# Optimization experiments

Measured on AMD Instinct MI355X. Metric: run time of the kernel, lower is better.

## Reference

```python
import jax, jax.numpy as jnp
import numpy as np

D_IN, D_HID, D_CLS, N_CLASSES = 1024, 256, 128, 4
CELL_IN = 512
N = 50000


def setup_inputs() -> dict:
    key = jax.random.key(0)
    ks = jax.random.split(key, 20)
    s = 0.02
    inp = {
        "x_path": jax.random.normal(ks[0], (1, N, D_IN), jnp.float32),
        "x_cell": jax.random.normal(ks[1], (1, N, CELL_IN), jnp.float32),
        # wsi_net / cell_net projections
        "wsi_w": jax.random.normal(ks[2], (D_IN, D_HID), jnp.float32) * s,
        "wsi_b": jnp.zeros((D_HID,), jnp.float32),
        "cell_w": jax.random.normal(ks[3], (CELL_IN, D_HID), jnp.float32) * s,
        "cell_b": jnp.zeros((D_HID,), jnp.float32),
        # cross-attention Q/K/V
        "wq_w": jax.random.normal(ks[4], (D_HID, D_HID), jnp.float32) * s,
        "wq_b": jnp.zeros((D_HID,), jnp.float32),
        "wk_w": jax.random.normal(ks[5], (D_HID, D_HID), jnp.float32) * s,
        "wk_b": jnp.zeros((D_HID,), jnp.float32),
        "wv_w": jax.random.normal(ks[6], (D_HID, D_HID), jnp.float32) * s,
        "wv_b": jnp.zeros((D_HID,), jnp.float32),
        # gated attention (L=D=256, n_classes=1)
        "aa_w": jax.random.normal(ks[7], (D_HID, D_HID), jnp.float32) * s,
        "aa_b": jnp.zeros((D_HID,), jnp.float32),
        "ab_w": jax.random.normal(ks[8], (D_HID, D_HID), jnp.float32) * s,
        "ab_b": jnp.zeros((D_HID,), jnp.float32),
        "ac_w": jax.random.normal(ks[9], (D_HID, 1), jnp.float32) * s,
        "ac_b": jnp.zeros((1,), jnp.float32),
        # classifier MLP
        "c1_w": jax.random.normal(ks[10], (D_HID, D_CLS), jnp.float32) * s,
        "c1_b": jnp.zeros((D_CLS,), jnp.float32),
        "c2_w": jax.random.normal(ks[11], (D_CLS, N_CLASSES), jnp.float32) * s,
        "c2_b": jnp.zeros((N_CLASSES,), jnp.float32),
    }
    return inp


def reference(x_path, x_cell, wsi_w, wsi_b, cell_w, cell_b,
              wq_w, wq_b, wk_w, wk_b, wv_w, wv_b,
              aa_w, aa_b, ab_w, ab_b, ac_w, ac_b,
              c1_w, c1_b, c2_w, c2_b):
    xp = x_path[0]            # (N, D_IN)
    xc = x_cell[0]            # (N, CELL_IN)
    # instance-level projections (dropout inactive at eval)
    h_path = jax.nn.relu(xp @ wsi_w + wsi_b)    # (N, d)
    h_cell = jax.nn.relu(xc @ cell_w + cell_b)  # (N, d)
    # cross attention with per-instance seq_len=1 (bmm over N singleton batches)
    q = h_cell @ wq_w + wq_b
    k = h_path @ wk_w + wk_b
    v = h_path @ wv_w + wv_b
    scores = (jnp.einsum('nd,nd->n', q, k) / jnp.sqrt(jnp.float32(q.shape[-1])))[:, None, None]  # (N,1,1)
    attn_w = jax.nn.softmax(scores, axis=-1)     # (N,1,1), trivially ones
    fused = attn_w[:, 0, :] * v                  # (N, d)
    # gated attention MIL pooling
    a = jnp.tanh(fused @ aa_w + aa_b)
    b = jax.nn.sigmoid(fused @ ab_w + ab_b)
    A = (a * b) @ ac_w + ac_b                    # (N, 1)
    A_t = A.T                                    # (1, N)
    pooled = jax.nn.softmax(A_t, axis=1) @ fused # (1, d)
    # classifier MLP
    risk = jax.nn.relu(pooled @ c1_w + c1_b) @ c2_w + c2_b  # (1, n_classes)
    return risk
```

## Files before the change

### kernel.cpp

```cpp
#include <hip/hip_runtime.h>
#include <hip/hip_bf16.h>
#include <math.h>

#define D_IN 1024
#define D_HID 256
#define D_CLS 128
#define N_CLASSES 4
#define N_INST 50000

#define ROWS 64
#define NBLK ((N_INST + ROWS - 1) / ROWS)
#define NB2 64
#define CHUNK ((NBLK + NB2 - 1) / NB2)
#define NEG_BIG (-1e30f)

typedef __attribute__((ext_vector_type(8))) short bf16x8;
typedef __attribute__((ext_vector_type(4))) float f32x4;

__device__ __forceinline__ short f2bf(float x) {
    __hip_bfloat16 h = __float2bfloat16(x);
    return *reinterpret_cast<short*>(&h);
}

__device__ __forceinline__ float fast_tanh(float x) {
    float e = __expf(2.f * x);
    return 1.f - 2.f * __builtin_amdgcn_rcpf(e + 1.f);
}
__device__ __forceinline__ float fast_sigmoid(float x) {
    return __builtin_amdgcn_rcpf(1.f + __expf(-x));
}

__device__ __forceinline__ bf16x8 load_cvt8(const float* __restrict__ p) {
    float4 a = *(const float4*)p;
    float4 b = *(const float4*)(p + 4);
    bf16x8 r;
    r[0] = f2bf(a.x); r[1] = f2bf(a.y); r[2] = f2bf(a.z); r[3] = f2bf(a.w);
    r[4] = f2bf(b.x); r[5] = f2bf(b.y); r[6] = f2bf(b.z); r[7] = f2bf(b.w);
    return r;
}

__global__ void convert_weights(const float* __restrict__ w1, const float* __restrict__ wv,
                                const float* __restrict__ wa, const float* __restrict__ wb,
                                __hip_bfloat16* __restrict__ w1t, __hip_bfloat16* __restrict__ wvt,
                                __hip_bfloat16* __restrict__ wat, __hip_bfloat16* __restrict__ wbt) {
    __shared__ __hip_bfloat16 T[64][68];
    int b = blockIdx.x, tid = threadIdx.x;
    const float* src; __hip_bfloat16* dst; int K, tr, tc;
    if (b < 64) { src = w1; dst = w1t; K = D_IN; tr = b >> 2; tc = b & 3; }
    else {
        int m = (b - 64) >> 4, t = (b - 64) & 15;
        src = (m == 0) ? wv : (m == 1) ? wa : wb;
        dst = (m == 0) ? wvt : (m == 1) ? wat : wbt;
        K = D_HID; tr = t >> 2; tc = t & 3;
    }
    int k0 = tr * 64, n0 = tc * 64;
#pragma unroll
    for (int p = 0; p < 4; p++) {
        int lin = p * 256 + tid;
        int r = lin >> 4;
        int c4 = (lin & 15) << 2;
        float4 v = *(const float4*)(src + (size_t)(k0 + r) * D_HID + n0 + c4);
        T[c4 + 0][r] = __float2bfloat16(v.x);
        T[c4 + 1][r] = __float2bfloat16(v.y);
        T[c4 + 2][r] = __float2bfloat16(v.z);
        T[c4 + 3][r] = __float2bfloat16(v.w);
    }
    __syncthreads();
#pragma unroll
    for (int p = 0; p < 4; p++) {
        int lin = p * 256 + tid;
        int n = lin >> 4;
        int kq = (lin & 15) << 2;
        ushort4 o;
        o.x = *(unsigned short*)&T[n][kq + 0];
        o.y = *(unsigned short*)&T[n][kq + 1];
        o.z = *(unsigned short*)&T[n][kq + 2];
        o.w = *(unsigned short*)&T[n][kq + 3];
        *(ushort4*)(dst + (size_t)(n0 + n) * K + k0 + kq) = o;
    }
}

__device__ __forceinline__ void gemm256(const __hip_bfloat16 (*S)[264],
                                        const __hip_bfloat16* __restrict__ Wt,
                                        int wave, int quad, int l16, f32x4 acc[4][4]) {
    f32x4 zero = {0.f, 0.f, 0.f, 0.f};
#pragma unroll
    for (int i = 0; i < 4; i++)
#pragma unroll
        for (int j = 0; j < 4; j++) acc[i][j] = zero;
#pragma unroll
    for (int ks = 0; ks < 8; ks++) {
        bf16x8 af[4];
#pragma unroll
        for (int rt = 0; rt < 4; rt++)
            af[rt] = *(const bf16x8*)&S[rt * 16 + l16][ks * 32 + quad * 8];
#pragma unroll
        for (int ct = 0; ct < 4; ct++) {
            bf16x8 bfv = *(const bf16x8*)(Wt + (size_t)(wave * 64 + ct * 16 + l16) * D_HID + ks * 32 + quad * 8);
#pragma unroll
            for (int rt = 0; rt < 4; rt++)
                acc[rt][ct] = __builtin_amdgcn_mfma_f32_16x16x32_bf16(af[rt], bfv, acc[rt][ct], 0, 0, 0);
        }
    }
}

__launch_bounds__(256, 2)
__global__ void mcat_main(const float* __restrict__ xp,
                          const __hip_bfloat16* __restrict__ w1t, const float* __restrict__ b1,
                          const __hip_bfloat16* __restrict__ wvt, const float* __restrict__ bv,
                          const __hip_bfloat16* __restrict__ wat, const float* __restrict__ ba,
                          const __hip_bfloat16* __restrict__ wbt, const float* __restrict__ bb,
                          const float* __restrict__ acw, const float* __restrict__ acb,
                          float* __restrict__ partials) {
    __shared__ __hip_bfloat16 Hs[ROWS][264];
    __shared__ __hip_bfloat16 Vs[ROWS][264];
    __shared__ float Apart[4][ROWS];
    __shared__ float ExpW[ROWS];

    const int tid  = threadIdx.x;
    const int wave = tid >> 6;
    const int lane = tid & 63;
    const int quad = lane >> 4;
    const int l16  = lane & 15;
    const int row0 = blockIdx.x * ROWS;

    f32x4 acc[4][4];
    f32x4 zero = {0.f, 0.f, 0.f, 0.f};
#pragma unroll
    for (int i = 0; i < 4; i++)
#pragma unroll
        for (int j = 0; j < 4; j++) acc[i][j] = zero;

    const float* xbase[4];
#pragma unroll
    for (int rt = 0; rt < 4; rt++) {
        int r = row0 + rt * 16 + l16;
        if (r > N_INST - 1) r = N_INST - 1;
        xbase[rt] = xp + (size_t)r * D_IN + quad * 8;
    }
    const __hip_bfloat16* wbase[4];
#pragma unroll
    for (int ct = 0; ct < 4; ct++)
        wbase[ct] = w1t + (size_t)(wave * 64 + ct * 16 + l16) * D_IN + quad * 8;

    for (int ko = 0; ko < 8; ko++) {
#pragma unroll
        for (int ki = 0; ki < 4; ki++) {
            const int kc = (ko * 4 + ki) * 32;
            bf16x8 af[4];
#pragma unroll
            for (int rt = 0; rt < 4; rt++)
                af[rt] = load_cvt8(xbase[rt] + kc);
#pragma unroll
            for (int ct = 0; ct < 4; ct++) {
                bf16x8 bfv = *(const bf16x8*)(wbase[ct] + kc);
#pragma unroll
                for (int rt = 0; rt < 4; rt++)
                    acc[rt][ct] = __builtin_amdgcn_mfma_f32_16x16x32_bf16(af[rt], bfv, acc[rt][ct], 0, 0, 0);
            }
        }
        __builtin_amdgcn_s_barrier();
    }

#pragma unroll
    for (int ct = 0; ct < 4; ct++) {
        int col = wave * 64 + ct * 16 + l16;
        float bias = b1[col];
#pragma unroll
        for (int rt = 0; rt < 4; rt++)
#pragma unroll
            for (int r = 0; r < 4; r++) {
                int row = rt * 16 + quad * 4 + r;
                float h = acc[rt][ct][r] + bias;
                Hs[row][col] = __float2bfloat16(fmaxf(h, 0.f));
            }
    }
    __syncthreads();

    gemm256(Hs, wvt, wave, quad, l16, acc);
#pragma unroll
    for (int ct = 0; ct < 4; ct++) {
        int col = wave * 64 + ct * 16 + l16;
        float bias = bv[col];
#pragma unroll
        for (int rt = 0; rt < 4; rt++)
#pragma unroll
            for (int r = 0; r < 4; r++) {
                int row = rt * 16 + quad * 4 + r;
                Vs[row][col] = __float2bfloat16(acc[rt][ct][r] + bias);
            }
    }
    __syncthreads();

    gemm256(Vs, wat, wave, quad, l16, acc);
#pragma unroll
    for (int ct = 0; ct < 4; ct++) {
        int col = wave * 64 + ct * 16 + l16;
        float bias = ba[col];
#pragma unroll
        for (int rt = 0; rt < 4; rt++)
#pragma unroll
            for (int r = 0; r < 4; r++) {
                int row = rt * 16 + quad * 4 + r;
                Hs[row][col] = __float2bfloat16(fast_tanh(acc[rt][ct][r] + bias));
            }
    }

    gemm256(Vs, wbt, wave, quad, l16, acc);
#pragma unroll
    for (int ct = 0; ct < 4; ct++) {
        int col = wave * 64 + ct * 16 + l16;
        float bias = bb[col];
#pragma unroll
        for (int rt = 0; rt < 4; rt++)
#pragma unroll
            for (int r = 0; r < 4; r++) {
                int row = rt * 16 + quad * 4 + r;
                float bval = fast_sigmoid(acc[rt][ct][r] + bias);
                float aval = __bfloat162float(Hs[row][col]);
                Hs[row][col] = __float2bfloat16(aval * bval);
            }
    }
    __syncthreads();

    {
        int r = tid & 63;
        int dg = tid >> 6;
        float s = 0.f;
#pragma unroll 8
        for (int d = 0; d < 64; d++) {
            int col = dg * 64 + d;
            s += __bfloat162float(Hs[r][col]) * acw[col];
        }
        Apart[dg][r] = s;
    }
    __syncthreads();

    if (tid < 64) {
        bool valid = (row0 + tid) < N_INST;
        float A = Apart[0][tid] + Apart[1][tid] + Apart[2][tid] + Apart[3][tid] + acb[0];
        if (!valid) A = NEG_BIG;
        float m = A;
#pragma unroll
        for (int off = 32; off > 0; off >>= 1) m = fmaxf(m, __shfl_xor(m, off));
        float e = valid ? __expf(A - m) : 0.f;
        ExpW[tid] = e;
        float ssum = e;
#pragma unroll
        for (int off = 32; off > 0; off >>= 1) ssum += __shfl_xor(ssum, off);
        if (tid == 0) {
            partials[(size_t)blockIdx.x * 258 + 0] = m;
            partials[(size_t)blockIdx.x * 258 + 1] = ssum;
        }
    }
    __syncthreads();
    {
        float p = 0.f;
#pragma unroll 8
        for (int n = 0; n < 64; n++)
            p += ExpW[n] * __bfloat162float(Vs[n][tid]);
        partials[(size_t)blockIdx.x * 258 + 2 + tid] = p;
    }
}

__global__ void mcat_fin_a(const float* __restrict__ p1, float* __restrict__ p2) {
    __shared__ float sm[1];
    int g = blockIdx.x, tid = threadIdx.x;
    int lo = g * CHUNK;
    int hi = lo + CHUNK; if (hi > NBLK) hi = NBLK;
    if (tid < 64) {
        float m = NEG_BIG;
        if (lo + tid < hi) m = p1[(size_t)(lo + tid) * 258];
#pragma unroll
        for (int off = 32; off > 0; off >>= 1) m = fmaxf(m, __shfl_xor(m, off));
        if (tid == 0) sm[0] = m;
    }
    __syncthreads();
    float M = sm[0];
    float p = 0.f, sacc = 0.f;
    for (int b = lo; b < hi; b++) {
        float sc = __expf(p1[(size_t)b * 258] - M);
        sacc += sc * p1[(size_t)b * 258 + 1];
        p += sc * p1[(size_t)b * 258 + 2 + tid];
    }
    if (tid == 0) {
        p2[(size_t)g * 258 + 0] = M;
        p2[(size_t)g * 258 + 1] = sacc;
    }
    p2[(size_t)g * 258 + 2 + tid] = p;
}

__global__ void mcat_fin_b(const float* __restrict__ p2,
                           const float* __restrict__ c1w, const float* __restrict__ c1b,
                           const float* __restrict__ c2w, const float* __restrict__ c2b,
                           float* __restrict__ out) {
    __shared__ float sm[2];
    __shared__ float sc[NB2];
    __shared__ float pooled[D_HID];
    __shared__ float r1[D_CLS];
    int tid = threadIdx.x;
    if (tid < 64) {
        float m = p2[(size_t)tid * 258];
#pragma unroll
        for (int off = 32; off > 0; off >>= 1) m = fmaxf(m, __shfl_xor(m, off));
        if (tid == 0) sm[0] = m;
    }
    __syncthreads();
    float M = sm[0];
    if (tid < 64) {
        float s = __expf(p2[(size_t)tid * 258] - M);
        sc[tid] = s;
        float Ssum = s * p2[(size_t)tid * 258 + 1];
#pragma unroll
        for (int off = 32; off > 0; off >>= 1) Ssum += __shfl_xor(Ssum, off);
        if (tid == 0) sm[1] = Ssum;
    }
    __syncthreads();
    float S = sm[1];
    float p = 0.f;
#pragma unroll 8
    for (int b = 0; b < NB2; b++)
        p += sc[b] * p2[(size_t)b * 258 + 2 + tid];
    pooled[tid] = p / S;
    __syncthreads();
    if (tid < D_CLS) {
        float acc = c1b[tid];
#pragma unroll 8
        for (int d = 0; d < D_HID; d++)
            acc += pooled[d] * c1w[(size_t)d * D_CLS + tid];
        r1[tid] = fmaxf(acc, 0.f);
    }
    __syncthreads();
    if (tid < N_CLASSES) {
        float acc = c2b[tid];
#pragma unroll 8
        for (int j = 0; j < D_CLS; j++)
            acc += r1[j] * c2w[(size_t)j * N_CLASSES + tid];
        out[tid] = acc;
    }
}

extern "C" void kernel_launch(void* const* d_in, const int* in_sizes, int n_in,
                              void* d_out, int out_size, void* d_ws, size_t ws_size,
                              hipStream_t stream) {
    const float* xp  = (const float*)d_in[0];
    const float* w1  = (const float*)d_in[2];
    const float* b1  = (const float*)d_in[3];
    const float* wv  = (const float*)d_in[10];
    const float* bv  = (const float*)d_in[11];
    const float* wa  = (const float*)d_in[12];
    const float* ba  = (const float*)d_in[13];
    const float* wb  = (const float*)d_in[14];
    const float* bb  = (const float*)d_in[15];
    const float* acw = (const float*)d_in[16];
    const float* acb = (const float*)d_in[17];
    const float* c1w = (const float*)d_in[18];
    const float* c1b = (const float*)d_in[19];
    const float* c2w = (const float*)d_in[20];
    const float* c2b = (const float*)d_in[21];
    float* out = (float*)d_out;

    char* ws = (char*)d_ws;
    __hip_bfloat16* w1t = (__hip_bfloat16*)(ws);
    __hip_bfloat16* wvt = (__hip_bfloat16*)(ws + 524288);
    __hip_bfloat16* wat = (__hip_bfloat16*)(ws + 655360);
    __hip_bfloat16* wbt = (__hip_bfloat16*)(ws + 786432);
    float* p1 = (float*)(ws + 917504);
    float* p2 = (float*)(ws + 917504 + 807024);

    hipLaunchKernelGGL(convert_weights, dim3(112), dim3(256), 0, stream,
                       w1, wv, wa, wb, w1t, wvt, wat, wbt);
    hipLaunchKernelGGL(mcat_main, dim3(NBLK), dim3(256), 0, stream,
                       xp, w1t, b1, wvt, bv, wat, ba, wbt, bb, acw, acb, p1);
    hipLaunchKernelGGL(mcat_fin_a, dim3(NB2), dim3(256), 0, stream, p1, p2);
    hipLaunchKernelGGL(mcat_fin_b, dim3(1), dim3(256), 0, stream,
                       p2, c1w, c1b, c2w, c2b, out);
}
```

Before: 545.7 us.

## Use 8 waves per block, pre-convert x to bf16, fuse gate reduction in registers

The main kernel moves from 4 waves to 8 waves per block, each owning 32 output columns, with launch bounds raised to (512,4) to increase occupancy. When the workspace is large enough, a separate kernel first converts x_path to bf16 so the main GEMM loads half the bytes. The gated-attention product and its dot with acw are now reduced in registers via shuffles instead of going through shared memory. The extra conversion pass adds a full fp32 read plus a bf16 write and read of x, which may cost more than the conversion work it removes. Each wave now also loads the full A tile on its own, doubling redundant x loads per block.

Result: slower. 623.9 us (+14.3%).

```diff
diff --git a/kernel.cpp b/kernel.cpp
--- a/kernel.cpp
+++ b/kernel.cpp
@@ -14,6 +14,15 @@
 #define CHUNK ((NBLK + NB2 - 1) / NB2)
 #define NEG_BIG (-1e30f)
 
+#define WS_W1T   0
+#define WS_WVT   524288
+#define WS_WAT   655360
+#define WS_WBT   786432
+#define WS_P1    917504
+#define WS_P2    1724528
+#define WS_XB    1835008
+#define WS_NEED  (WS_XB + (size_t)N_INST * D_IN * 2)
+
 typedef __attribute__((ext_vector_type(8))) short bf16x8;
 typedef __attribute__((ext_vector_type(4))) float f32x4;
 
@@ -21,7 +30,6 @@
     __hip_bfloat16 h = __float2bfloat16(x);
     return *reinterpret_cast<short*>(&h);
 }
-
 __device__ __forceinline__ float fast_tanh(float x) {
     float e = __expf(2.f * x);
     return 1.f - 2.f * __builtin_amdgcn_rcpf(e + 1.f);
@@ -29,7 +37,6 @@
 __device__ __forceinline__ float fast_sigmoid(float x) {
     return __builtin_amdgcn_rcpf(1.f + __expf(-x));
 }
-
 __device__ __forceinline__ bf16x8 load_cvt8(const float* __restrict__ p) {
     float4 a = *(const float4*)p;
     float4 b = *(const float4*)(p + 4);
@@ -37,6 +44,13 @@
     r[0] = f2bf(a.x); r[1] = f2bf(a.y); r[2] = f2bf(a.z); r[3] = f2bf(a.w);
     r[4] = f2bf(b.x); r[5] = f2bf(b.y); r[6] = f2bf(b.z); r[7] = f2bf(b.w);
     return r;
+}
+
+__global__ __launch_bounds__(256) void convert_x(const float* __restrict__ xp,
+                                                 __hip_bfloat16* __restrict__ xb) {
+    size_t i = ((size_t)blockIdx.x * 256 + threadIdx.x) * 8;
+    bf16x8 v = load_cvt8(xp + i);
+    *(bf16x8*)(xb + i) = v;
 }
 
 __global__ void convert_weights(const float* __restrict__ w1, const float* __restrict__ wv,
@@ -80,32 +94,32 @@
     }
 }
 
-__device__ __forceinline__ void gemm256(const __hip_bfloat16 (*S)[264],
-                                        const __hip_bfloat16* __restrict__ Wt,
-                                        int wave, int quad, int l16, f32x4 acc[4][4]) {
+__device__ __forceinline__ void gemm256_w8(const __hip_bfloat16 (*S)[264],
+                                           const __hip_bfloat16* __restrict__ Wt,
+                                           int colbase, int quad, int l16, f32x4 acc[4][2]) {
     f32x4 zero = {0.f, 0.f, 0.f, 0.f};
 #pragma unroll
-    for (int i = 0; i < 4; i++)
-#pragma unroll
-        for (int j = 0; j < 4; j++) acc[i][j] = zero;
+    for (int i = 0; i < 4; i++) { acc[i][0] = zero; acc[i][1] = zero; }
+    const __hip_bfloat16* w0 = Wt + (size_t)(colbase + l16) * D_HID + quad * 8;
+    const __hip_bfloat16* w1 = w0 + 16 * D_HID;
 #pragma unroll
     for (int ks = 0; ks < 8; ks++) {
         bf16x8 af[4];
 #pragma unroll
         for (int rt = 0; rt < 4; rt++)
             af[rt] = *(const bf16x8*)&S[rt * 16 + l16][ks * 32 + quad * 8];
-#pragma unroll
-        for (int ct = 0; ct < 4; ct++) {
-            bf16x8 bfv = *(const bf16x8*)(Wt + (size_t)(wave * 64 + ct * 16 + l16) * D_HID + ks * 32 + quad * 8);
-#pragma unroll
-            for (int rt = 0; rt < 4; rt++)
-                acc[rt][ct] = __builtin_amdgcn_mfma_f32_16x16x32_bf16(af[rt], bfv, acc[rt][ct], 0, 0, 0);
+        bf16x8 b0 = *(const bf16x8*)(w0 + ks * 32);
+        bf16x8 b1 = *(const bf16x8*)(w1 + ks * 32);
+#pragma unroll
+        for (int rt = 0; rt < 4; rt++) {
+            acc[rt][0] = __builtin_amdgcn_mfma_f32_16x16x32_bf16(af[rt], b0, acc[rt][0], 0, 0, 0);
+            acc[rt][1] = __builtin_amdgcn_mfma_f32_16x16x32_bf16(af[rt], b1, acc[rt][1], 0, 0, 0);
         }
     }
 }
 
-__launch_bounds__(256, 2)
-__global__ void mcat_main(const float* __restrict__ xp,
+template <bool XBF16>
+__global__ __launch_bounds__(512, 4) void mcat_main(const void* __restrict__ xsrc,
                           const __hip_bfloat16* __restrict__ w1t, const float* __restrict__ b1,
                           const __hip_bfloat16* __restrict__ wvt, const float* __restrict__ bv,
                           const __hip_bfloat16* __restrict__ wat, const float* __restrict__ ba,
@@ -114,7 +128,7 @@
                           float* __restrict__ partials) {
     __shared__ __hip_bfloat16 Hs[ROWS][264];
     __shared__ __hip_bfloat16 Vs[ROWS][264];
-    __shared__ float Apart[4][ROWS];
+    __shared__ float Apart[8][ROWS];
     __shared__ float ExpW[ROWS];
 
     const int tid  = threadIdx.x;
@@ -122,65 +136,59 @@
     const int lane = tid & 63;
     const int quad = lane >> 4;
     const int l16  = lane & 15;
+    const int colbase = wave * 32;
     const int row0 = blockIdx.x * ROWS;
 
-    f32x4 acc[4][4];
+    f32x4 acc[4][2];
     f32x4 zero = {0.f, 0.f, 0.f, 0.f};
 #pragma unroll
-    for (int i = 0; i < 4; i++)
-#pragma unroll
-        for (int j = 0; j < 4; j++) acc[i][j] = zero;
-
-    const float* xbase[4];
+    for (int i = 0; i < 4; i++) { acc[i][0] = zero; acc[i][1] = zero; }
+
+    const __hip_bfloat16* xb_base[4];
+    const float* xf_base[4];
 #pragma unroll
     for (int rt = 0; rt < 4; rt++) {
         int r = row0 + rt * 16 + l16;
         if (r > N_INST - 1) r = N_INST - 1;
-        xbase[rt] = xp + (size_t)r * D_IN + quad * 8;
-    }
-    const __hip_bfloat16* wbase[4];
-#pragma unroll
-    for (int ct = 0; ct < 4; ct++)
-        wbase[ct] = w1t + (size_t)(wave * 64 + ct * 16 + l16) * D_IN + quad * 8;
-
-    for (int ko = 0; ko < 8; ko++) {
-#pragma unroll
-        for (int ki = 0; ki < 4; ki++) {
-            const int kc = (ko * 4 + ki) * 32;
-            bf16x8 af[4];
-#pragma unroll
-            for (int rt = 0; rt < 4; rt++)
-                af[rt] = load_cvt8(xbase[rt] + kc);
-#pragma unroll
-            for (int ct = 0; ct < 4; ct++) {
-                bf16x8 bfv = *(const bf16x8*)(wbase[ct] + kc);
-#pragma unroll
-                for (int rt = 0; rt < 4; rt++)
-                    acc[rt][ct] = __builtin_amdgcn_mfma_f32_16x16x32_bf16(af[rt], bfv, acc[rt][ct], 0, 0, 0);
-            }
+        if (XBF16) xb_base[rt] = (const __hip_bfloat16*)xsrc + (size_t)r * D_IN + quad * 8;
+        else       xf_base[rt] = (const float*)xsrc + (size_t)r * D_IN + quad * 8;
+    }
+    const __hip_bfloat16* wb0 = w1t + (size_t)(colbase + l16) * D_IN + quad * 8;
+    const __hip_bfloat16* wb1 = wb0 + 16 * D_IN;
+
+    for (int kc = 0; kc < D_IN; kc += 32) {
+        bf16x8 af[4];
+#pragma unroll
+        for (int rt = 0; rt < 4; rt++)
+            af[rt] = XBF16 ? *(const bf16x8*)(xb_base[rt] + kc)
+                           : load_cvt8(xf_base[rt] + kc);
+        bf16x8 b0 = *(const bf16x8*)(wb0 + kc);
+        bf16x8 b1 = *(const bf16x8*)(wb1 + kc);
+#pragma unroll
+        for (int rt = 0; rt < 4; rt++) {
+            acc[rt][0] = __builtin_amdgcn_mfma_f32_16x16x32_bf16(af[rt], b0, acc[rt][0], 0, 0, 0);
+            acc[rt][1] = __builtin_amdgcn_mfma_f32_16x16x32_bf16(af[rt], b1, acc[rt][1], 0, 0, 0);
         }
-        __builtin_amdgcn_s_barrier();
-    }
-
-#pragma unroll
-    for (int ct = 0; ct < 4; ct++) {
-        int col = wave * 64 + ct * 16 + l16;
+    }
+
+#pragma unroll
+    for (int ct = 0; ct < 2; ct++) {
+        int col = colbase + ct * 16 + l16;
         float bias = b1[col];
 #pragma unroll
         for (int rt = 0; rt < 4; rt++)
 #pragma unroll
             for (int r = 0; r < 4; r++) {
                 int row = rt * 16 + quad * 4 + r;
-                float h = acc[rt][ct][r] + bias;
-                Hs[row][col] = __float2bfloat16(fmaxf(h, 0.f));
+                Hs[row][col] = __float2bfloat16(fmaxf(acc[rt][ct][r] + bias, 0.f));
             }
     }
     __syncthreads();
 
-    gemm256(Hs, wvt, wave, quad, l16, acc);
-#pragma unroll
-    for (int ct = 0; ct < 4; ct++) {
-        int col = wave * 64 + ct * 16 + l16;
+    gemm256_w8(Hs, wvt, colbase, quad, l16, acc);
+#pragma unroll
+    for (int ct = 0; ct < 2; ct++) {
+        int col = colbase + ct * 16 + l16;
         float bias = bv[col];
 #pragma unroll
         for (int rt = 0; rt < 4; rt++)
@@ -192,53 +200,55 @@
     }
     __syncthreads();
 
-    gemm256(Vs, wat, wave, quad, l16, acc);
-#pragma unroll
-    for (int ct = 0; ct < 4; ct++) {
-        int col = wave * 64 + ct * 16 + l16;
-        float bias = ba[col];
+    float a_reg[4][2][4];
+    gemm256_w8(Vs, wat, colbase, quad, l16, acc);
+#pragma unroll
+    for (int ct = 0; ct < 2; ct++) {
+        float bias = ba[colbase + ct * 16 + l16];
+#pragma unroll
+        for (int rt = 0; rt < 4; rt++)
+#pragma unroll
+            for (int r = 0; r < 4; r++)
+                a_reg[rt][ct][r] = fast_tanh(acc[rt][ct][r] + bias);
+    }
+
+    gemm256_w8(Vs, wbt, colbase, quad, l16, acc);
+    {
+        float acw0 = acw[colbase + l16];
+        float acw1 = acw[colbase + 16 + l16];
+        float bias0 = bb[colbase + l16];
+        float bias1 = bb[colbase + 16 + l16];
+        float sp[4][4];
 #pragma unroll
         for (int rt = 0; rt < 4; rt++)
 #pragma unroll
             for (int r = 0; r < 4; r++) {
-                int row = rt * 16 + quad * 4 + r;
-                Hs[row][col] = __float2bfloat16(fast_tanh(acc[rt][ct][r] + bias));
+                float g0 = a_reg[rt][0][r] * fast_sigmoid(acc[rt][0][r] + bias0);
+                float g1 = a_reg[rt][1][r] * fast_sigmoid(acc[rt][1][r] + bias1);
+                sp[rt][r] = g0 * acw0 + g1 * acw1;
             }
-    }
-
-    gemm256(Vs, wbt, wave, quad, l16, acc);
-#pragma unroll
-    for (int ct = 0; ct < 4; ct++) {
-        int col = wave * 64 + ct * 16 + l16;
-        float bias = bb[col];
-#pragma unroll
-        for (int rt = 0; rt < 4; rt++)
-#pragma unroll
-            for (int r = 0; r < 4; r++) {
-                int row = rt * 16 + quad * 4 + r;
-                float bval = fast_sigmoid(acc[rt][ct][r] + bias);
-                float aval = __bfloat162float(Hs[row][col]);
-                Hs[row][col] = __float2bfloat16(aval * bval);
-            }
-    }
-    __syncthreads();
-
-    {
-        int r = tid & 63;
-        int dg = tid >> 6;
-        float s = 0.f;
-#pragma unroll 8
-        for (int d = 0; d < 64; d++) {
-            int col = dg * 64 + d;
-            s += __bfloat162float(Hs[r][col]) * acw[col];
+#pragma unroll
+        for (int off = 1; off < 16; off <<= 1)
+#pragma unroll
+            for (int rt = 0; rt < 4; rt++)
+#pragma unroll
+                for (int r = 0; r < 4; r++)
+                    sp[rt][r] += __shfl_xor(sp[rt][r], off, 16);
+        if (l16 == 0) {
+#pragma unroll
+            for (int rt = 0; rt < 4; rt++)
+#pragma unroll
+                for (int r = 0; r < 4; r++)
+                    Apart[wave][rt * 16 + quad * 4 + r] = sp[rt][r];
         }
-        Apart[dg][r] = s;
     }
     __syncthreads();
 
     if (tid < 64) {
         bool valid = (row0 + tid) < N_INST;
-        float A = Apart[0][tid] + Apart[1][tid] + Apart[2][tid] + Apart[3][tid] + acb[0];
+        float A = acb[0];
+#pragma unroll
+        for (int w = 0; w < 8; w++) A += Apart[w][tid];
         if (!valid) A = NEG_BIG;
         float m = A;
 #pragma unroll
@@ -254,7 +264,7 @@
         }
     }
     __syncthreads();
-    {
+    if (tid < 256) {
         float p = 0.f;
 #pragma unroll 8
         for (int n = 0; n < 64; n++)
@@ -361,17 +371,26 @@
     float* out = (float*)d_out;
 
     char* ws = (char*)d_ws;
-    __hip_bfloat16* w1t = (__hip_bfloat16*)(ws);
-    __hip_bfloat16* wvt = (__hip_bfloat16*)(ws + 524288);
-    __hip_bfloat16* wat = (__hip_bfloat16*)(ws + 655360);
-    __hip_bfloat16* wbt = (__hip_bfloat16*)(ws + 786432);
-    float* p1 = (float*)(ws + 917504);
-    float* p2 = (float*)(ws + 917504 + 807024);
+    __hip_bfloat16* w1t = (__hip_bfloat16*)(ws + WS_W1T);
+    __hip_bfloat16* wvt = (__hip_bfloat16*)(ws + WS_WVT);
+    __hip_bfloat16* wat = (__hip_bfloat16*)(ws + WS_WAT);
+    __hip_bfloat16* wbt = (__hip_bfloat16*)(ws + WS_WBT);
+    float* p1 = (float*)(ws + WS_P1);
+    float* p2 = (float*)(ws + WS_P2);
+    __hip_bfloat16* xb = (__hip_bfloat16*)(ws + WS_XB);
+
+    const bool big = ws_size >= WS_NEED;
 
     hipLaunchKernelGGL(convert_weights, dim3(112), dim3(256), 0, stream,
                        w1, wv, wa, wb, w1t, wvt, wat, wbt);
-    hipLaunchKernelGGL(mcat_main, dim3(NBLK), dim3(256), 0, stream,
-                       xp, w1t, b1, wvt, bv, wat, ba, wbt, bb, acw, acb, p1);
+    if (big) {
+        hipLaunchKernelGGL(convert_x, dim3(N_INST * D_IN / 8 / 256), dim3(256), 0, stream, xp, xb);
+        hipLaunchKernelGGL((mcat_main<true>), dim3(NBLK), dim3(512), 0, stream,
+                           (const void*)xb, w1t, b1, wvt, bv, wat, ba, wbt, bb, acw, acb, p1);
+    } else {
+        hipLaunchKernelGGL((mcat_main<false>), dim3(NBLK), dim3(512), 0, stream,
+                           (const void*)xp, w1t, b1, wvt, bv, wat, ba, wbt, bb, acw, acb, p1);
+    }
     hipLaunchKernelGGL(mcat_fin_a, dim3(NB2), dim3(256), 0, stream, p1, p2);
     hipLaunchKernelGGL(mcat_fin_b, dim3(1), dim3(256), 0, stream,
                        p2, c1w, c1b, c2w, c2b, out);
```
